# Performance work log

Hardware: AMD Instinct MI355X
Metric: run time of the kernel (lower is better)

Reference implementation:

```python
import jax, jax.numpy as jnp
import numpy as np

N_WIRES = 4
DEPTH = 2
BN_EPS = 1e-5


def _rx(theta):
    c = jnp.cos(theta / 2).astype(jnp.complex64)
    s = jnp.sin(theta / 2).astype(jnp.complex64)
    return jnp.stack([jnp.stack([c, -1j * s], -1),
                      jnp.stack([-1j * s, c], -1)], -2)


def _ry(theta):
    c = jnp.cos(theta / 2).astype(jnp.complex64)
    s = jnp.sin(theta / 2).astype(jnp.complex64)
    return jnp.stack([jnp.stack([c, -s], -1),
                      jnp.stack([s, c], -1)], -2)


def _rz(theta):
    e = jnp.exp(-1j * theta.astype(jnp.complex64) / 2)
    z = jnp.zeros_like(e)
    return jnp.stack([jnp.stack([e, z], -1),
                      jnp.stack([z, jnp.conj(e)], -1)], -2)


def _apply_1q(state, U, wire):
    # state: [B,2,2,2,2]; U: [2,2] (shared) or [B,2,2] (per-sample)
    ax = 1 + wire
    st = jnp.moveaxis(state, ax, -1)
    if U.ndim == 3:
        st = jnp.einsum('bij,b...j->b...i', U, st)
    else:
        st = jnp.einsum('ij,...j->...i', U, st)
    return jnp.moveaxis(st, -1, ax)


def _apply_cnot(state, c, t):
    axc, axt = 1 + c, 1 + t
    st = jnp.moveaxis(state, (axc, axt), (-2, -1))
    st = jnp.stack([st[..., 0, :], st[..., 1, ::-1]], axis=-2)
    return jnp.moveaxis(st, (-2, -1), (axc, axt))


def _circuit(pooled, enc_w, enc_b, var_params):
    B = pooled.shape[0]
    angles = pooled @ enc_w.T + enc_b  # [B,4]
    # |0000> state, [B,2,2,2,2]
    state = jnp.zeros((B, 16), jnp.complex64).at[:, 0].set(1.0)
    state = state.reshape((B,) + (2,) * N_WIRES)
    for i in range(N_WIRES):
        state = _apply_1q(state, _rx(angles[:, i]), i)  # batched RX encoding
    for d in range(DEPTH):
        for i in range(N_WIRES):
            state = _apply_1q(state, _rx(var_params[d, i, 0]), i)
            state = _apply_1q(state, _ry(var_params[d, i, 1]), i)
            state = _apply_1q(state, _rz(var_params[d, i, 2]), i)
        for i in range(N_WIRES - 1):
            state = _apply_cnot(state, i, i + 1)
        state = _apply_cnot(state, N_WIRES - 1, 0)
    probs = jnp.real(state * jnp.conj(state))  # [B,2,2,2,2]
    zs = []
    for i in range(N_WIRES):
        other = tuple(a for a in range(1, 1 + N_WIRES) if a != 1 + i)
        p = probs.sum(other)  # [B,2]
        zs.append(p[:, 0] - p[:, 1])
    return jnp.stack(zs, -1)  # [B,4]


def setup_inputs() -> dict:
    key = jax.random.key(0)
    ks = jax.random.split(key, 4)
    B = 65536
    return {
        'x': jax.random.normal(ks[0], (B, 1, 24, 24), jnp.float32),
        'enc_w': jax.random.normal(ks[1], (4, 16), jnp.float32) * 0.25,
        'enc_b': jax.random.normal(ks[2], (4,), jnp.float32) * 0.25,
        'var_params': jax.random.normal(ks[3], (DEPTH, N_WIRES, 3), jnp.float32),
        'gamma': jnp.ones((4,), jnp.float32),
        'beta': jnp.zeros((4,), jnp.float32),
    }


def reference(x, enc_w, enc_b, var_params, gamma, beta):
    B = x.shape[0]
    # avg_pool2d kernel 6 on [B,1,24,24] -> [B,1,4,4] -> [B,16]
    pooled = x.reshape(B, 1, 4, 6, 4, 6).mean((3, 5)).reshape(B, 16)
    z = _circuit(pooled, enc_w, enc_b, var_params)  # [B,4] analytic expvals
    # BatchNorm1d (training mode: biased batch statistics)
    mean = z.mean(0)
    var = z.var(0)
    return (z - mean) / jnp.sqrt(var + BN_EPS) * gamma + beta
```

## Files before the change

### kernel.cpp

```cpp
#include <hip/hip_runtime.h>


__device__ __forceinline__ void apply_rx(float* sr, float* si, int bit, float c, float s) {
    const int m = 1 << bit;
#pragma unroll
    for (int idx = 0; idx < 16; ++idx) {
        if (idx & m) continue;
        const int j = idx | m;
        float a0r = sr[idx], a0i = si[idx], a1r = sr[j], a1i = si[j];
        sr[idx] = c * a0r + s * a1i;
        si[idx] = c * a0i - s * a1r;
        sr[j]   = c * a1r + s * a0i;
        si[j]   = c * a1i - s * a0r;
    }
}

__device__ __forceinline__ void apply_ry(float* sr, float* si, int bit, float c, float s) {
    const int m = 1 << bit;
#pragma unroll
    for (int idx = 0; idx < 16; ++idx) {
        if (idx & m) continue;
        const int j = idx | m;
        float a0r = sr[idx], a0i = si[idx], a1r = sr[j], a1i = si[j];
        sr[idx] = c * a0r - s * a1r;
        si[idx] = c * a0i - s * a1i;
        sr[j]   = s * a0r + c * a1r;
        si[j]   = s * a0i + c * a1i;
    }
}

__device__ __forceinline__ void apply_rz(float* sr, float* si, int bit, float c, float s) {
    const int m = 1 << bit;
#pragma unroll
    for (int idx = 0; idx < 16; ++idx) {
        if (idx & m) continue;
        const int j = idx | m;
        float a0r = sr[idx], a0i = si[idx], a1r = sr[j], a1i = si[j];
        sr[idx] = c * a0r + s * a0i;
        si[idx] = c * a0i - s * a0r;
        sr[j]   = c * a1r - s * a1i;
        si[j]   = c * a1i + s * a1r;
    }
}

__device__ __forceinline__ void apply_cnot(float* sr, float* si, int cw, int tw) {
    const int cb = 3 - cw, tb = 3 - tw;
#pragma unroll
    for (int idx = 0; idx < 16; ++idx) {
        if (((idx >> cb) & 1) && !((idx >> tb) & 1)) {
            const int j = idx | (1 << tb);
            float tr = sr[idx]; sr[idx] = sr[j]; sr[j] = tr;
            float ti = si[idx]; si[idx] = si[j]; si[j] = ti;
        }
    }
}


__device__ __forceinline__ void pool_circuit(
    const float4* __restrict__ x,
    const float* __restrict__ enc_w,
    const float* __restrict__ enc_b,
    const float* __restrict__ var_params,
    int s, int q, float z[4])
{
    float pacc[4] = {0.0f, 0.0f, 0.0f, 0.0f};
    const float4* xs = x + (size_t)s * 144 + q * 36;
#pragma unroll
    for (int j = 0; j < 36; ++j) {
        const float4 v = xs[j];
        pacc[((4 * j + 0) % 24) / 6] += v.x;
        pacc[((4 * j + 1) % 24) / 6] += v.y;
        pacc[((4 * j + 2) % 24) / 6] += v.z;
        pacc[((4 * j + 3) % 24) / 6] += v.w;
    }

    float pa[4];
#pragma unroll
    for (int i = 0; i < 4; ++i) {
        const float* wr = enc_w + i * 16 + q * 4;
        pa[i] = (wr[0] * pacc[0] + wr[1] * pacc[1] +
                 wr[2] * pacc[2] + wr[3] * pacc[3]) * (1.0f / 36.0f);
    }
    float av[4];
#pragma unroll
    for (int i = 0; i < 4; ++i) {
        float v = pa[i];
        v += __shfl_xor(v, 1, 64);
        v += __shfl_xor(v, 2, 64);
        av[i] = v + enc_b[i];
    }

    float gc[24], gs[24];
#pragma unroll
    for (int i = 0; i < 24; ++i) {
        float sn, cs;
        __sincosf(0.5f * var_params[i], &sn, &cs);
        gc[i] = cs; gs[i] = sn;
    }

    float sr[16], si[16];
#pragma unroll
    for (int i = 0; i < 16; ++i) { sr[i] = 0.0f; si[i] = 0.0f; }
    sr[0] = 1.0f;

#pragma unroll
    for (int w = 0; w < 4; ++w) {
        float sn, cs;
        __sincosf(0.5f * av[w], &sn, &cs);
        apply_rx(sr, si, 3 - w, cs, sn);
    }

#pragma unroll
    for (int d = 0; d < 2; ++d) {
#pragma unroll
        for (int w = 0; w < 4; ++w) {
            const int base = d * 12 + w * 3;
            apply_rx(sr, si, 3 - w, gc[base + 0], gs[base + 0]);
            apply_ry(sr, si, 3 - w, gc[base + 1], gs[base + 1]);
            apply_rz(sr, si, 3 - w, gc[base + 2], gs[base + 2]);
        }
        apply_cnot(sr, si, 0, 1);
        apply_cnot(sr, si, 1, 2);
        apply_cnot(sr, si, 2, 3);
        apply_cnot(sr, si, 3, 0);
    }

    float pr16[16];
#pragma unroll
    for (int i = 0; i < 16; ++i) pr16[i] = sr[i] * sr[i] + si[i] * si[i];

#pragma unroll
    for (int w = 0; w < 4; ++w) {
        const int bit = 3 - w;
        float acc = 0.0f;
#pragma unroll
        for (int i = 0; i < 16; ++i)
            acc += ((i >> bit) & 1) ? -pr16[i] : pr16[i];
        z[w] = acc;
    }
}

__global__ __launch_bounds__(256, 4) void fused_pc(
    const float4* __restrict__ x,
    const float* __restrict__ enc_w, const float* __restrict__ enc_b,
    const float* __restrict__ var_params,
    float* __restrict__ out_z,
    float* __restrict__ partials)
{
    __shared__ float red[4 * 8];
    const int t = threadIdx.x;
    const int s = blockIdx.x * 64 + (t >> 2);
    const int q = t & 3;

    float z[4];
    pool_circuit(x, enc_w, enc_b, var_params, s, q, z);
    out_z[blockIdx.x * 256 + t] = z[q];

    float vals[8] = {z[0], z[1], z[2], z[3],
                     z[0] * z[0], z[1] * z[1], z[2] * z[2], z[3] * z[3]};
#pragma unroll
    for (int j = 0; j < 8; ++j) {
        float v = vals[j];
#pragma unroll
        for (int off = 32; off >= 1; off >>= 1)
            v += __shfl_down(v, off, 64);
        if ((t & 63) == 0) red[(t >> 6) * 8 + j] = v;
    }
    __syncthreads();
    if (t < 8)
        partials[blockIdx.x * 8 + t] =
            0.25f * (red[t] + red[8 + t] + red[16 + t] + red[24 + t]);
}

__global__ __launch_bounds__(256) void bn_kernel(
    float4* __restrict__ io,
    const float* __restrict__ partials,
    const float* __restrict__ gamma,
    const float* __restrict__ beta,
    int nPartialRows, int B)
{
    __shared__ float stats[8];
    const int t = threadIdx.x;

    if (t < 64) {
        float part[8];
#pragma unroll
        for (int j = 0; j < 8; ++j) part[j] = 0.0f;
        for (int r = t; r < nPartialRows; r += 64) {
            const float* row = partials + r * 8;
#pragma unroll
            for (int j = 0; j < 8; ++j) part[j] += row[j];
        }
#pragma unroll
        for (int j = 0; j < 8; ++j) {
            float v = part[j];
#pragma unroll
            for (int off = 32; off >= 1; off >>= 1)
                v += __shfl_down(v, off, 64);
            if (t == 0) stats[j] = v;
        }
    }
    __syncthreads();

    const int b = blockIdx.x * 256 + t;
    const float invB = 1.0f / (float)B;
    const float4 z4 = io[b];
    const float zz[4] = {z4.x, z4.y, z4.z, z4.w};

    float res[4];
#pragma unroll
    for (int i = 0; i < 4; ++i) {
        const float mean = stats[i] * invB;
        float var = stats[4 + i] * invB - mean * mean;
        var = fmaxf(var, 0.0f);
        const float scale = gamma[i] * rsqrtf(var + 1e-5f);
        res[i] = (zz[i] - mean) * scale + beta[i];
    }
    io[b] = make_float4(res[0], res[1], res[2], res[3]);
}

extern "C" void kernel_launch(void* const* d_in, const int* in_sizes, int n_in,
                              void* d_out, int out_size, void* d_ws, size_t ws_size,
                              hipStream_t stream) {
    const float4* x = (const float4*)d_in[0];
    const float* enc_w = (const float*)d_in[1];
    const float* enc_b = (const float*)d_in[2];
    const float* var_params = (const float*)d_in[3];
    const float* gamma = (const float*)d_in[4];
    const float* beta = (const float*)d_in[5];

    int B = in_sizes[0] / 576;
    float* out = (float*)d_out;
    float* partials = (float*)d_ws;

    const int nBlocks = B / 64;

    fused_pc<<<nBlocks, 256, 0, stream>>>(x, enc_w, enc_b, var_params, out, partials);
    bn_kernel<<<B / 256, 256, 0, stream>>>((float4*)out, partials, gamma, beta,
                                           nBlocks, B);
}
```

Baseline: 239.0 us.

## Interleave per-sample pooling loads across quad lanes for coalesced access

Each of the four threads serving a sample now reads float4s at stride 4 (lane q takes elements q, q+4, …), so adjacent lanes touch adjacent addresses instead of separate contiguous 36-float4 chunks. Each thread keeps all 16 pooled partials, reduces them across the quad with shuffles, and computes the full 16x4 encoder matvec itself. The launch_bounds occupancy hint of 4 is dropped. The change costs more shuffles, more registers and redundant matvec work per thread in exchange for better coalesced global loads.

```diff
diff --git a/kernel.cpp b/kernel.cpp
--- a/kernel.cpp
+++ b/kernel.cpp
@@ -56,38 +56,68 @@
 }
 
 
-__device__ __forceinline__ void pool_circuit(
+__global__ __launch_bounds__(256) void fused_stream(
     const float4* __restrict__ x,
     const float* __restrict__ enc_w,
     const float* __restrict__ enc_b,
     const float* __restrict__ var_params,
-    int s, int q, float z[4])
+    float* __restrict__ out_z,
+    float* __restrict__ partials)
 {
-    float pacc[4] = {0.0f, 0.0f, 0.0f, 0.0f};
-    const float4* xs = x + (size_t)s * 144 + q * 36;
+    __shared__ float red[4 * 8];
+
+    const int t = threadIdx.x;
+    const int q = t & 3;
+    const int s = blockIdx.x * 64 + (t >> 2);
+
+    const float4* xsq = x + (size_t)s * 144 + q;
+
+    int cb0 = 4 * q;
+    int cb1 = 16 + 4 * q; if (cb1 >= 24) cb1 -= 24;
+    int cb2 = 8 + 4 * q;
+    int pcs[3][4];
+#pragma unroll
+    for (int c = 0; c < 4; ++c) {
+        pcs[0][c] = (cb0 + c) / 6;
+        pcs[1][c] = (cb1 + c) / 6;
+        pcs[2][c] = (cb2 + c) / 6;
+    }
+
+    float pacc[16];
+#pragma unroll
+    for (int i = 0; i < 16; ++i) pacc[i] = 0.0f;
+
 #pragma unroll
     for (int j = 0; j < 36; ++j) {
-        const float4 v = xs[j];
-        pacc[((4 * j + 0) % 24) / 6] += v.x;
-        pacc[((4 * j + 1) % 24) / 6] += v.y;
-        pacc[((4 * j + 2) % 24) / 6] += v.z;
-        pacc[((4 * j + 3) % 24) / 6] += v.w;
-    }
-
-    float pa[4];
+        const float4 v = xsq[4 * j];
+        const int r4 = (j / 9) * 4;
+        const int m = j % 3;
+        const float e[4] = {v.x, v.y, v.z, v.w};
+#pragma unroll
+        for (int c = 0; c < 4; ++c) {
+#pragma unroll
+            for (int p = 0; p < 4; ++p)
+                pacc[r4 + p] += (pcs[m][c] == p) ? e[c] : 0.0f;
+        }
+    }
+
+    float pooled[16];
+#pragma unroll
+    for (int k = 0; k < 16; ++k) {
+        float p = pacc[k];
+        p += __shfl_xor(p, 1, 64);
+        p += __shfl_xor(p, 2, 64);
+        pooled[k] = p * (1.0f / 36.0f);
+    }
+
+    float av[4];
 #pragma unroll
     for (int i = 0; i < 4; ++i) {
-        const float* wr = enc_w + i * 16 + q * 4;
-        pa[i] = (wr[0] * pacc[0] + wr[1] * pacc[1] +
-                 wr[2] * pacc[2] + wr[3] * pacc[3]) * (1.0f / 36.0f);
-    }
-    float av[4];
-#pragma unroll
-    for (int i = 0; i < 4; ++i) {
-        float v = pa[i];
-        v += __shfl_xor(v, 1, 64);
-        v += __shfl_xor(v, 2, 64);
-        av[i] = v + enc_b[i];
+        float a = enc_b[i];
+#pragma unroll
+        for (int k = 0; k < 16; ++k)
+            a += enc_w[i * 16 + k] * pooled[k];
+        av[i] = a;
     }
 
     float gc[24], gs[24];
@@ -129,6 +159,7 @@
 #pragma unroll
     for (int i = 0; i < 16; ++i) pr16[i] = sr[i] * sr[i] + si[i] * si[i];
 
+    float z[4];
 #pragma unroll
     for (int w = 0; w < 4; ++w) {
         const int bit = 3 - w;
@@ -138,22 +169,7 @@
             acc += ((i >> bit) & 1) ? -pr16[i] : pr16[i];
         z[w] = acc;
     }
-}
-
-__global__ __launch_bounds__(256, 4) void fused_pc(
-    const float4* __restrict__ x,
-    const float* __restrict__ enc_w, const float* __restrict__ enc_b,
-    const float* __restrict__ var_params,
-    float* __restrict__ out_z,
-    float* __restrict__ partials)
-{
-    __shared__ float red[4 * 8];
-    const int t = threadIdx.x;
-    const int s = blockIdx.x * 64 + (t >> 2);
-    const int q = t & 3;
-
-    float z[4];
-    pool_circuit(x, enc_w, enc_b, var_params, s, q, z);
+
     out_z[blockIdx.x * 256 + t] = z[q];
 
     float vals[8] = {z[0], z[1], z[2], z[3],
@@ -229,13 +245,14 @@
     const float* gamma = (const float*)d_in[4];
     const float* beta = (const float*)d_in[5];
 
-    int B = in_sizes[0] / 576;
+    const int B = in_sizes[0] / 576;
     float* out = (float*)d_out;
     float* partials = (float*)d_ws;
 
     const int nBlocks = B / 64;
 
-    fused_pc<<<nBlocks, 256, 0, stream>>>(x, enc_w, enc_b, var_params, out, partials);
+    fused_stream<<<nBlocks, 256, 0, stream>>>(x, enc_w, enc_b, var_params,
+                                              out, partials);
     bn_kernel<<<B / 256, 256, 0, stream>>>((float4*)out, partials, gamma, beta,
                                            nBlocks, B);
 }
```

Result: no change. 234.5 us (-1.9%).
